# Kernel tuning notes

Hardware: AMD Instinct MI355X
Metric: run time of the kernel (lower is better)

The kernel has to match this reference:

```python
import jax, jax.numpy as jnp
import numpy as np

HID = 1024
NH = 16
HD = HID // NH  # 64
RANK = 16
B, L = 2, 2048


def setup_inputs() -> dict:
    key = jax.random.key(0)
    ks = jax.random.split(key, 9)
    s = 0.02
    return {
        "x": jax.random.normal(ks[0], (B, L, HID), dtype=jnp.float32),
        "Wq": jax.random.normal(ks[1], (HID, HID), dtype=jnp.float32) * s,
        "Wk": jax.random.normal(ks[2], (HID, HID), dtype=jnp.float32) * s,
        "Wv": jax.random.normal(ks[3], (HID, HID), dtype=jnp.float32) * s,
        "Wg": jax.random.normal(ks[4], (HID, HID), dtype=jnp.float32) * s,
        "Wgk1": jax.random.normal(ks[5], (HID, RANK), dtype=jnp.float32) * s,
        "Wgk2": jax.random.normal(ks[6], (RANK, HID), dtype=jnp.float32) * s,
        "bgk2": jnp.zeros((HID,), dtype=jnp.float32),
        "gamma": jnp.ones((HID,), dtype=jnp.float32),
        "beta": jnp.zeros((HID,), dtype=jnp.float32),
        "Wout": jax.random.normal(ks[7], (HID, HID), dtype=jnp.float32) * s,
    }


def reference(x, Wq, Wk, Wv, Wg, Wgk1, Wgk2, bgk2, gamma, beta, Wout):
    Bb, Ll, Hid = x.shape
    H, Dh = NH, HD
    # projections -> [B, L, H, Dh]
    q = (x @ Wq).reshape(Bb, Ll, H, Dh)
    k = (x @ Wk).reshape(Bb, Ll, H, Dh)
    v = (x @ Wv).reshape(Bb, Ll, H, Dh)
    gk = (jax.nn.log_sigmoid((x @ Wgk1) @ Wgk2 + bgk2) / 16.0).reshape(Bb, Ll, H, Dh)

    # time-major for scan: [L, B, H, Dh]
    qT = jnp.transpose(q, (1, 0, 2, 3))
    kT = jnp.transpose(k, (1, 0, 2, 3))
    vT = jnp.transpose(v, (1, 0, 2, 3))
    gT = jnp.transpose(gk, (1, 0, 2, 3))

    def step(state, inp):
        qt, kt, vt, gt = inp  # each [B, H, Dh]
        gate = jnp.exp(gt)
        # state[b,h,v_dim,k_dim]; gate applied along v_dim (matches torch code)
        state = state * gate[..., None] + vt[..., None] * kt[..., None, :]
        out_t = jnp.einsum('bhvk,bhk->bhv', state, qt)
        return state, out_t

    state0 = jnp.zeros((Bb, H, Dh, Dh), dtype=x.dtype)
    _, outs = jax.lax.scan(step, state0, (qT, kT, vT, gT))  # outs: [L, B, H, Dh]
    out = jnp.transpose(outs, (1, 0, 2, 3)).reshape(Bb, Ll, Hid)

    # LayerNorm over total_dim
    mu = out.mean(-1, keepdims=True)
    var = out.var(-1, keepdims=True)
    out = (out - mu) / jnp.sqrt(var + 1e-5) * gamma + beta

    # output gate + projection (dropout = identity in eval)
    out = out * jax.nn.silu(x @ Wg)
    return out @ Wout
```

## Files before the change

### kernel.cpp

```cpp
#include <hip/hip_runtime.h>
#include <cstdint>
#include <cstddef>

#define HIDS 1024
#define NHEAD 16
#define HDIM 64
#define LSEQ 2048
#define BBATCH 2
#define NROW (BBATCH * LSEQ)
#define CHUNK 64
#define NCHUNK (LSEQ / CHUNK)
#define RANK 16

typedef short short8 __attribute__((ext_vector_type(8)));
typedef float floatx4 __attribute__((ext_vector_type(4)));

__device__ __forceinline__ ushort f2bf(float f) {
  uint32_t u = __float_as_uint(f);
  uint32_t r = (u + 0x7fffu + ((u >> 16) & 1u)) >> 16;
  return (ushort)r;
}
__device__ __forceinline__ float bf2f(ushort u) {
  return __uint_as_float(((uint32_t)u) << 16);
}
__device__ __forceinline__ float logsig16(float z) {
  return (fminf(z, 0.f) - __logf(1.f + __expf(-fabsf(z)))) * (1.f / 16.f);
}

__device__ __forceinline__ void async_copy16(const void* g, void* l) {
  __builtin_amdgcn_global_load_lds(
      (const __attribute__((address_space(1))) void*)g,
      (__attribute__((address_space(3))) void*)l, 16, 0, 0);
}

__global__ __launch_bounds__(256) void prep_kernel(
    const float* __restrict__ x, ushort* __restrict__ xbf,
    const float* __restrict__ W0, const float* __restrict__ W1,
    const float* __restrict__ W2, const float* __restrict__ W3,
    const float* __restrict__ W4, ushort* __restrict__ T0,
    ushort* __restrict__ T1, ushort* __restrict__ T2, ushort* __restrict__ T3,
    ushort* __restrict__ T4) {
  __shared__ float sbuf[64 * 65];
  const int bid = blockIdx.x;
  const int tid = threadIdx.x;

  if (bid < 4096) {
    const int i = bid * 256 + tid;
    float4 f = *(const float4*)(x + (size_t)i * 4);
    ushort4 o;
    o.x = f2bf(f.x); o.y = f2bf(f.y); o.z = f2bf(f.z); o.w = f2bf(f.w);
    *(ushort4*)(xbf + (size_t)i * 4) = o;
  } else {
    const int w = bid - 4096;
    const int z = w >> 8, rem = w & 255;
    const float* W = (z == 0) ? W0 : (z == 1) ? W1 : (z == 2) ? W2
                     : (z == 3) ? W3 : W4;
    ushort* T = (z == 0) ? T0 : (z == 1) ? T1 : (z == 2) ? T2
                : (z == 3) ? T3 : T4;
    const int k0 = (rem >> 4) * 64, n0 = (rem & 15) * 64;
    const int r = tid >> 2, c4 = (tid & 3) * 16;
#pragma unroll
    for (int i = 0; i < 4; ++i) {
      float4 f = *(const float4*)(W + (size_t)(k0 + r) * HIDS + n0 + c4 + i * 4);
      sbuf[r * 65 + c4 + i * 4 + 0] = f.x;
      sbuf[r * 65 + c4 + i * 4 + 1] = f.y;
      sbuf[r * 65 + c4 + i * 4 + 2] = f.z;
      sbuf[r * 65 + c4 + i * 4 + 3] = f.w;
    }
    __syncthreads();
    const int n = tid >> 2, kc = (tid & 3) * 16;
#pragma unroll
    for (int i = 0; i < 4; ++i) {
      int kk = kc + i * 4;
      ushort4 o;
      o.x = f2bf(sbuf[(kk + 0) * 65 + n]);
      o.y = f2bf(sbuf[(kk + 1) * 65 + n]);
      o.z = f2bf(sbuf[(kk + 2) * 65 + n]);
      o.w = f2bf(sbuf[(kk + 3) * 65 + n]);
      *(ushort4*)(T + (size_t)(n0 + n) * HIDS + k0 + kk) = o;
    }
  }
}

#define XSTR 1040
__global__ __launch_bounds__(256) void xr_kernel(
    const ushort* __restrict__ xbf, const float* __restrict__ Wgk1,
    float* __restrict__ xr) {
  __shared__ float sW1[HIDS * RANK];
  __shared__ ushort sX[16 * XSTR];
  const int tid = threadIdx.x;
  const int r0 = blockIdx.x * 16;
#pragma unroll
  for (int j = 0; j < 16; ++j) {
    const int idx = j * 1024 + tid * 4;
    *(float4*)&sW1[idx] = *(const float4*)(Wgk1 + idx);
  }
#pragma unroll
  for (int j = 0; j < 8; ++j) {
    const int e = j * 2048 + tid * 8;
    const int rr = e >> 10, kk = e & 1023;
    *(short8*)&sX[rr * XSTR + kk] =
        *(const short8*)(xbf + (size_t)(r0 + rr) * HIDS + kk);
  }
  __syncthreads();
  const int r = tid >> 4, n = tid & 15;
  float acc = 0.f;
  for (int k8 = 0; k8 < HIDS; k8 += 8) {
    short8 xv = *(const short8*)&sX[r * XSTR + k8];
#pragma unroll
    for (int i = 0; i < 8; ++i)
      acc = fmaf(bf2f((ushort)xv[i]), sW1[(k8 + i) * RANK + n], acc);
  }
  xr[(size_t)(r0 + r) * RANK + n] = acc;
}

__global__ __launch_bounds__(256) void proj4_kernel(
    const ushort* __restrict__ xbf, const ushort* __restrict__ Wtq,
    const ushort* __restrict__ Wtk, const ushort* __restrict__ Wtv,
    const ushort* __restrict__ Wtg, ushort* __restrict__ qb,
    ushort* __restrict__ kb, ushort* __restrict__ vb, ushort* __restrict__ gb) {
  const int bxz = blockIdx.x;
  const int z = bxz & 3;
  const int bx = bxz >> 2;
  const ushort* Bt = (z == 0) ? Wtq : (z == 1) ? Wtk : (z == 2) ? Wtv : Wtg;
  ushort* C = (z == 0) ? qb : (z == 1) ? kb : (z == 2) ? vb : gb;
  __shared__ ushort As[2][128 * 32];
  __shared__ ushort Bs[2][128 * 32];
  const int tid = threadIdx.x;
  const int wave = tid >> 6, lane = tid & 63;
  const int wm = (wave >> 1) * 64, wn = (wave & 1) * 64;
  const int bm = blockIdx.y * 128, bn = bx * 128;
  const int lrow = tid >> 2;
  const int lk8 = ((((tid & 3) - ((tid >> 3) & 3)) & 3)) * 8;
  const ushort* Ag = xbf + (size_t)(bm + lrow) * HIDS + lk8;
  const ushort* Bg = Bt + (size_t)(bn + lrow) * HIDS + lk8;
  char* A0 = (char*)&As[0][0] + tid * 16;
  char* A1 = (char*)&As[1][0] + tid * 16;
  char* B0 = (char*)&Bs[0][0] + tid * 16;
  char* B1 = (char*)&Bs[1][0] + tid * 16;

  floatx4 acc[4][4];
#pragma unroll
  for (int i = 0; i < 4; ++i)
#pragma unroll
    for (int j = 0; j < 4; ++j) acc[i][j] = (floatx4){0.f, 0.f, 0.f, 0.f};

  const int fm = lane & 15, quad = lane >> 4;
  const int sq8 = ((quad + (fm >> 1)) & 3) * 8;

  for (int k0 = 0; k0 < HIDS; k0 += 64) {
    __syncthreads();
    async_copy16(Ag + k0, A0);
    async_copy16(Ag + (size_t)64 * HIDS + k0, A0 + 4096);
    async_copy16(Ag + k0 + 32, A1);
    async_copy16(Ag + (size_t)64 * HIDS + k0 + 32, A1 + 4096);
    async_copy16(Bg + k0, B0);
    async_copy16(Bg + (size_t)64 * HIDS + k0, B0 + 4096);
    async_copy16(Bg + k0 + 32, B1);
    async_copy16(Bg + (size_t)64 * HIDS + k0 + 32, B1 + 4096);
    __syncthreads();

#pragma unroll
    for (int ks = 0; ks < 2; ++ks) {
      short8 af[4], bfr[4];
#pragma unroll
      for (int i = 0; i < 4; ++i)
        af[i] = *(const short8*)&As[ks][(wm + i * 16 + fm) * 32 + sq8];
#pragma unroll
      for (int j = 0; j < 4; ++j)
        bfr[j] = *(const short8*)&Bs[ks][(wn + j * 16 + fm) * 32 + sq8];
#pragma unroll
      for (int i = 0; i < 4; ++i)
#pragma unroll
        for (int j = 0; j < 4; ++j)
          acc[i][j] = __builtin_amdgcn_mfma_f32_16x16x32_bf16(af[i], bfr[j],
                                                              acc[i][j], 0, 0, 0);
    }
  }

#pragma unroll
  for (int i = 0; i < 4; ++i) {
    const int row0 = bm + wm + i * 16 + quad * 4;
#pragma unroll
    for (int j = 0; j < 4; ++j) {
      const int col = bn + wn + j * 16 + fm;
#pragma unroll
      for (int r = 0; r < 4; ++r)
        C[(size_t)(row0 + r) * HIDS + col] = f2bf(acc[i][j][r]);
    }
  }
}

__global__ __launch_bounds__(256) void gemm_out_kernel(
    const ushort* __restrict__ A, const ushort* __restrict__ Bt,
    float* __restrict__ C) {
  __shared__ ushort As[2][128 * 32];
  __shared__ ushort Bs[2][128 * 32];
  const int tid = threadIdx.x;
  const int wave = tid >> 6, lane = tid & 63;
  const int wm = (wave >> 1) * 64, wn = (wave & 1) * 64;
  const int fm = lane & 15, quad = lane >> 4;
  const int sq8 = ((quad + (fm >> 1)) & 3) * 8;
  const int bm = blockIdx.y * 128, bn = blockIdx.x * 128;
  const int lrow = tid >> 2;
  const int lk8 = ((((tid & 3) - ((tid >> 3) & 3)) & 3)) * 8;
  const ushort* Ag = A + (size_t)(bm + lrow) * HIDS + lk8;
  const ushort* Bg = Bt + (size_t)(bn + lrow) * HIDS + lk8;
  char* A0 = (char*)&As[0][0] + tid * 16;
  char* A1 = (char*)&As[1][0] + tid * 16;
  char* B0 = (char*)&Bs[0][0] + tid * 16;
  char* B1 = (char*)&Bs[1][0] + tid * 16;

  floatx4 acc[4][4];
#pragma unroll
  for (int i = 0; i < 4; ++i)
#pragma unroll
    for (int j = 0; j < 4; ++j) acc[i][j] = (floatx4){0.f, 0.f, 0.f, 0.f};

  for (int k0 = 0; k0 < HIDS; k0 += 64) {
    __syncthreads();
    async_copy16(Ag + k0, A0);
    async_copy16(Ag + (size_t)64 * HIDS + k0, A0 + 4096);
    async_copy16(Ag + k0 + 32, A1);
    async_copy16(Ag + (size_t)64 * HIDS + k0 + 32, A1 + 4096);
    async_copy16(Bg + k0, B0);
    async_copy16(Bg + (size_t)64 * HIDS + k0, B0 + 4096);
    async_copy16(Bg + k0 + 32, B1);
    async_copy16(Bg + (size_t)64 * HIDS + k0 + 32, B1 + 4096);
    __syncthreads();

#pragma unroll
    for (int ks = 0; ks < 2; ++ks) {
      short8 af[4], bfr[4];
#pragma unroll
      for (int i = 0; i < 4; ++i)
        af[i] = *(const short8*)&As[ks][(wm + i * 16 + fm) * 32 + sq8];
#pragma unroll
      for (int j = 0; j < 4; ++j)
        bfr[j] = *(const short8*)&Bs[ks][(wn + j * 16 + fm) * 32 + sq8];
#pragma unroll
      for (int i = 0; i < 4; ++i)
#pragma unroll
        for (int j = 0; j < 4; ++j)
          acc[i][j] = __builtin_amdgcn_mfma_f32_16x16x32_bf16(af[i], bfr[j],
                                                              acc[i][j], 0, 0, 0);
    }
  }

#pragma unroll
  for (int i = 0; i < 4; ++i) {
    const int row0 = bm + wm + i * 16 + quad * 4;
#pragma unroll
    for (int j = 0; j < 4; ++j) {
      const int col = bn + wn + j * 16 + fm;
#pragma unroll
      for (int r = 0; r < 4; ++r)
        C[(size_t)(row0 + r) * HIDS + col] = acc[i][j][r];
    }
  }
}

#define SP 72
#define SGS 68

__global__ __launch_bounds__(256) void sdelta_kernel(
    const ushort* __restrict__ k, const ushort* __restrict__ v,
    const float* __restrict__ xr, const float* __restrict__ Wgk2,
    const float* __restrict__ bgk2, ushort* __restrict__ Sdelta,
    float* __restrict__ Lam, ushort* __restrict__ Vtg,
    ushort* __restrict__ Eb) {
  const int bid = blockIdx.x;
  const int c = bid & 31, bh = bid >> 5;
  const int b = bh >> 4, h = bh & 15;
  const int tid = threadIdx.x;
  const int lane = tid & 63, wave = tid >> 6;
  const int fm = lane & 15, quad = lane >> 4;
  const int wm2 = (wave >> 1) * 32, wn2 = (wave & 1) * 32;

  __shared__ ushort sKt[64 * SP];
  __shared__ ushort sVt[64 * SP];
  __shared__ float sG[64 * SGS];
  __shared__ float sW2[RANK * 64];

  const size_t base = ((size_t)b * LSEQ + (size_t)c * CHUNK) * HIDS + (size_t)h * HDIM;
  const int r = tid >> 2, c0 = (tid & 3) * 16;
  const size_t gb = base + (size_t)r * HIDS + c0;

  {
    const int wr = tid >> 4, wc = (tid & 15) * 4;
    *(float4*)&sW2[wr * 64 + wc] =
        *(const float4*)(Wgk2 + (size_t)wr * HIDS + h * HDIM + wc);
  }
  float xrr[16];
  {
    const size_t xrow = ((size_t)b * LSEQ + (size_t)c * CHUNK + r) * RANK;
#pragma unroll
    for (int m = 0; m < 4; ++m)
      *(float4*)&xrr[m * 4] = *(const float4*)(xr + xrow + m * 4);
  }
  float bias[16];
#pragma unroll
  for (int m = 0; m < 4; ++m)
    *(float4*)&bias[m * 4] = *(const float4*)(bgk2 + h * HDIM + c0 + m * 4);
  __syncthreads();

#pragma unroll
  for (int i = 0; i < 16; ++i) {
    float z = bias[i];
#pragma unroll
    for (int t2 = 0; t2 < 16; ++t2)
      z = fmaf(xrr[t2], sW2[t2 * 64 + c0 + i], z);
    sG[r * SGS + c0 + i] = logsig16(z);
  }
  const int pr = (tid >> 3) * 2, pc = (tid & 7) * 8;
  const size_t pb = base + (size_t)pr * HIDS + pc;
  short8 ka = *(const short8*)(k + pb);
  short8 kb2 = *(const short8*)(k + pb + HIDS);
  short8 va = *(const short8*)(v + pb);
  short8 vb2 = *(const short8*)(v + pb + HIDS);
  __syncthreads();

  const int vcol = tid & 63, qtr = tid >> 6;
  {
    float run = 0.f;
#pragma unroll
    for (int i = 0; i < 16; ++i) {
      int idx = (qtr * 16 + i) * SGS + vcol;
      run += sG[idx];
      sG[idx] = run;
    }
  }
  __syncthreads();
  float pre = 0.f;
  for (int j = 0; j < qtr; ++j) pre += sG[(j * 16 + 15) * SGS + vcol];
  __syncthreads();
#pragma unroll
  for (int i = 0; i < 16; ++i) sG[(qtr * 16 + i) * SGS + vcol] += pre;
  __syncthreads();

  {
    ushort eb[16];
#pragma unroll
    for (int i = 0; i < 16; ++i) eb[i] = f2bf(__expf(sG[r * SGS + c0 + i]));
    *(short8*)(Eb + gb) = *(short8*)&eb[0];
    *(short8*)(Eb + gb + 8) = *(short8*)&eb[8];
  }

#pragma unroll
  for (int i = 0; i < 8; ++i) {
    ushort2 kk;
    kk.x = (ushort)ka[i];
    kk.y = (ushort)kb2[i];
    *(ushort2*)&sKt[(pc + i) * SP + pr] = kk;
    float Ga = sG[pr * SGS + pc + i];
    float Gb2 = sG[(pr + 1) * SGS + pc + i];
    ushort2 vv;
    vv.x = f2bf(bf2f((ushort)va[i]) * __expf(-Ga));
    vv.y = f2bf(bf2f((ushort)vb2[i]) * __expf(-Gb2));
    *(ushort2*)&sVt[(pc + i) * SP + pr] = vv;
  }
  __syncthreads();

  {
    const size_t vb3 = (size_t)(bh * NCHUNK + c) * (HDIM * HDIM);
    *(short8*)(Vtg + vb3 + (size_t)r * HDIM + c0) = *(const short8*)&sVt[r * SP + c0];
    *(short8*)(Vtg + vb3 + (size_t)r * HDIM + c0 + 8) =
        *(const short8*)&sVt[r * SP + c0 + 8];
  }

  if (tid < 64)
    Lam[(size_t)(bh * NCHUNK + c) * HDIM + tid] = __expf(sG[63 * SGS + tid]);

  floatx4 accD[2][2];
#pragma unroll
  for (int i = 0; i < 2; ++i)
#pragma unroll
    for (int j = 0; j < 2; ++j) accD[i][j] = (floatx4){0.f, 0.f, 0.f, 0.f};
#pragma unroll
  for (int ks = 0; ks < 2; ++ks) {
    short8 av[2], bk[2];
#pragma unroll
    for (int i = 0; i < 2; ++i)
      av[i] = *(const short8*)&sVt[(wm2 + i * 16 + fm) * SP + ks * 32 + quad * 8];
#pragma unroll
    for (int j = 0; j < 2; ++j)
      bk[j] = *(const short8*)&sKt[(wn2 + j * 16 + fm) * SP + ks * 32 + quad * 8];
#pragma unroll
    for (int i = 0; i < 2; ++i)
#pragma unroll
      for (int j = 0; j < 2; ++j)
        accD[i][j] = __builtin_amdgcn_mfma_f32_16x16x32_bf16(av[i], bk[j],
                                                             accD[i][j], 0, 0, 0);
  }
  const size_t sbase = (size_t)(bh * NCHUNK + c) * (HDIM * HDIM);
#pragma unroll
  for (int i = 0; i < 2; ++i) {
    const int m0 = wm2 + i * 16 + quad * 4;
    float lam[4];
#pragma unroll
    for (int rr = 0; rr < 4; ++rr) lam[rr] = __expf(sG[63 * SGS + m0 + rr]);
#pragma unroll
    for (int j = 0; j < 2; ++j) {
      const int n = wn2 + j * 16 + fm;
#pragma unroll
      for (int rr = 0; rr < 4; ++rr)
        Sdelta[sbase + (size_t)(m0 + rr) * HDIM + n] = f2bf(accD[i][j][rr] * lam[rr]);
    }
  }
}

__global__ __launch_bounds__(256) void state_scan_kernel(
    const ushort* __restrict__ Sdelta, const float* __restrict__ Lam,
    ushort* __restrict__ Sprev) {
  const int bh = blockIdx.x >> 3;
  const int sl = blockIdx.x & 7;
  const int tid = threadIdx.x;
  const int e0 = sl * 512 + tid;
  float S0 = 0.f, S1 = 0.f;

  float pd0[2], pd1[2], pl0[2], pl1[2];
#pragma unroll
  for (int s = 0; s < 2; ++s) {
    size_t nb = (size_t)(bh * NCHUNK + s) * (HDIM * HDIM);
    size_t nl = (size_t)(bh * NCHUNK + s) * HDIM;
    pd0[s] = bf2f(Sdelta[nb + e0]);
    pd1[s] = bf2f(Sdelta[nb + e0 + 256]);
    pl0[s] = Lam[nl + (e0 >> 6)];
    pl1[s] = Lam[nl + ((e0 + 256) >> 6)];
  }

  for (int c = 0; c < NCHUNK; ++c) {
    const int s = c & 1;
    float cd0 = pd0[s], cd1 = pd1[s], cl0 = pl0[s], cl1 = pl1[s];
    if (c + 2 < NCHUNK) {
      size_t nb = (size_t)(bh * NCHUNK + c + 2) * (HDIM * HDIM);
      size_t nl = (size_t)(bh * NCHUNK + c + 2) * HDIM;
      pd0[s] = bf2f(Sdelta[nb + e0]);
      pd1[s] = bf2f(Sdelta[nb + e0 + 256]);
      pl0[s] = Lam[nl + (e0 >> 6)];
      pl1[s] = Lam[nl + ((e0 + 256) >> 6)];
    }
    size_t ob = (size_t)(bh * NCHUNK + c) * (HDIM * HDIM);
    Sprev[ob + e0] = f2bf(S0);
    Sprev[ob + e0 + 256] = f2bf(S1);
    S0 = fmaf(S0, cl0, cd0);
    S1 = fmaf(S1, cl1, cd1);
  }
}

__global__ __launch_bounds__(256) void chunk_fused_kernel(
    const ushort* __restrict__ q, const ushort* __restrict__ k,
    const ushort* __restrict__ Vtg, const ushort* __restrict__ Eb,
    const ushort* __restrict__ Sprev, ushort* __restrict__ att) {
  const int bid = blockIdx.x;
  const int c = bid & 31, bh = bid >> 5;
  const int b = bh >> 4, h = bh & 15;
  const int tid = threadIdx.x;
  const int lane = tid & 63, wave = tid >> 6;
  const int fm = lane & 15, quad = lane >> 4;
  const int wm2 = (wave >> 1) * 32, wn2 = (wave & 1) * 32;

  __shared__ ushort sQ[64 * SP];
  __shared__ ushort sK[64 * SP];
  __shared__ ushort sVt[64 * SP];
  __shared__ ushort sA[64 * SP];
  ushort* sSp = sK;

  const size_t base = ((size_t)b * LSEQ + (size_t)c * CHUNK) * HIDS + (size_t)h * HDIM;
  const size_t sbase = (size_t)(bh * NCHUNK + c) * (HDIM * HDIM);
  const int r = tid >> 2, c0 = (tid & 3) * 16;
  const size_t gb = base + (size_t)r * HIDS + c0;
  short8 sp0 = *(const short8*)(Sprev + sbase + (size_t)r * HDIM + c0);
  short8 sp1 = *(const short8*)(Sprev + sbase + (size_t)r * HDIM + c0 + 8);
  *(short8*)&sQ[r * SP + c0] = *(const short8*)(q + gb);
  *(short8*)&sQ[r * SP + c0 + 8] = *(const short8*)(q + gb + 8);
  *(short8*)&sK[r * SP + c0] = *(const short8*)(k + gb);
  *(short8*)&sK[r * SP + c0 + 8] = *(const short8*)(k + gb + 8);
  *(short8*)&sVt[r * SP + c0] = *(const short8*)(Vtg + sbase + (size_t)r * HDIM + c0);
  *(short8*)&sVt[r * SP + c0 + 8] =
      *(const short8*)(Vtg + sbase + (size_t)r * HDIM + c0 + 8);
  __syncthreads();

  floatx4 accS[2][2];
#pragma unroll
  for (int i = 0; i < 2; ++i)
#pragma unroll
    for (int j = 0; j < 2; ++j) accS[i][j] = (floatx4){0.f, 0.f, 0.f, 0.f};
#pragma unroll
  for (int ks = 0; ks < 2; ++ks) {
    short8 a[2], bb[2];
#pragma unroll
    for (int i = 0; i < 2; ++i)
      a[i] = *(const short8*)&sQ[(wm2 + i * 16 + fm) * SP + ks * 32 + quad * 8];
#pragma unroll
    for (int j = 0; j < 2; ++j)
      bb[j] = *(const short8*)&sK[(wn2 + j * 16 + fm) * SP + ks * 32 + quad * 8];
#pragma unroll
    for (int i = 0; i < 2; ++i)
#pragma unroll
      for (int j = 0; j < 2; ++j)
        accS[i][j] = __builtin_amdgcn_mfma_f32_16x16x32_bf16(a[i], bb[j],
                                                             accS[i][j], 0, 0, 0);
  }
  __syncthreads();

#pragma unroll
  for (int i = 0; i < 2; ++i)
#pragma unroll
    for (int j = 0; j < 2; ++j) {
      const int t0 = wm2 + i * 16 + quad * 4;
      const int s = wn2 + j * 16 + fm;
#pragma unroll
      for (int rr = 0; rr < 4; ++rr) {
        float val = (s <= t0 + rr) ? accS[i][j][rr] : 0.f;
        sA[(t0 + rr) * SP + s] = f2bf(val);
      }
    }
  *(short8*)&sSp[r * SP + c0] = sp0;
  *(short8*)&sSp[r * SP + c0 + 8] = sp1;
  __syncthreads();

  floatx4 acc[2][2];
#pragma unroll
  for (int i = 0; i < 2; ++i)
#pragma unroll
    for (int j = 0; j < 2; ++j) acc[i][j] = (floatx4){0.f, 0.f, 0.f, 0.f};
#pragma unroll
  for (int ks = 0; ks < 2; ++ks) {
    short8 aa[2], aq[2], bv[2], bs[2];
#pragma unroll
    for (int i = 0; i < 2; ++i) {
      aa[i] = *(const short8*)&sA[(wm2 + i * 16 + fm) * SP + ks * 32 + quad * 8];
      aq[i] = *(const short8*)&sQ[(wm2 + i * 16 + fm) * SP + ks * 32 + quad * 8];
    }
#pragma unroll
    for (int j = 0; j < 2; ++j) {
      bv[j] = *(const short8*)&sVt[(wn2 + j * 16 + fm) * SP + ks * 32 + quad * 8];
      bs[j] = *(const short8*)&sSp[(wn2 + j * 16 + fm) * SP + ks * 32 + quad * 8];
    }
#pragma unroll
    for (int i = 0; i < 2; ++i)
#pragma unroll
      for (int j = 0; j < 2; ++j) {
        acc[i][j] = __builtin_amdgcn_mfma_f32_16x16x32_bf16(aa[i], bv[j],
                                                            acc[i][j], 0, 0, 0);
        acc[i][j] = __builtin_amdgcn_mfma_f32_16x16x32_bf16(aq[i], bs[j],
                                                            acc[i][j], 0, 0, 0);
      }
  }
#pragma unroll
  for (int i = 0; i < 2; ++i)
#pragma unroll
    for (int j = 0; j < 2; ++j) {
      const int m0 = wm2 + i * 16 + quad * 4;
      const int n = wn2 + j * 16 + fm;
#pragma unroll
      for (int rr = 0; rr < 4; ++rr) {
        const size_t idx = base + (size_t)(m0 + rr) * HIDS + n;
        att[idx] = f2bf(acc[i][j][rr] * bf2f(Eb[idx]));
      }
    }
}

__global__ __launch_bounds__(256) void ln_gate_kernel(const ushort* __restrict__ att,
                                                      const ushort* __restrict__ g,
                                                      const float* __restrict__ gamma,
                                                      const float* __restrict__ beta,
                                                      ushort* __restrict__ ybf) {
  const int row = blockIdx.x;
  const int tid = threadIdx.x;
  ushort4 au = *(const ushort4*)(att + (size_t)row * HIDS + tid * 4);
  float ax = bf2f(au.x), ay = bf2f(au.y), az = bf2f(au.z), aw = bf2f(au.w);
  float s = ax + ay + az + aw;
  float ss = ax * ax + ay * ay + az * az + aw * aw;
#pragma unroll
  for (int off = 32; off; off >>= 1) {
    s += __shfl_down(s, off);
    ss += __shfl_down(ss, off);
  }
  __shared__ float rs[4], rss[4];
  const int wid = tid >> 6;
  if ((tid & 63) == 0) { rs[wid] = s; rss[wid] = ss; }
  __syncthreads();
  const float mean = (rs[0] + rs[1] + rs[2] + rs[3]) * (1.f / HIDS);
  const float ex2 = (rss[0] + rss[1] + rss[2] + rss[3]) * (1.f / HIDS);
  const float rstd = rsqrtf(ex2 - mean * mean + 1e-5f);

  float4 ga = *(const float4*)(gamma + tid * 4);
  float4 be = *(const float4*)(beta + tid * 4);
  ushort4 gu = *(const ushort4*)(g + (size_t)row * HIDS + tid * 4);
  float gx = bf2f(gu.x), gy = bf2f(gu.y), gz = bf2f(gu.z), gw = bf2f(gu.w);
  float4 o;
  o.x = ((ax - mean) * rstd * ga.x + be.x) * (gx / (1.f + __expf(-gx)));
  o.y = ((ay - mean) * rstd * ga.y + be.y) * (gy / (1.f + __expf(-gy)));
  o.z = ((az - mean) * rstd * ga.z + be.z) * (gz / (1.f + __expf(-gz)));
  o.w = ((aw - mean) * rstd * ga.w + be.w) * (gw / (1.f + __expf(-gw)));
  ushort4 ob;
  ob.x = f2bf(o.x); ob.y = f2bf(o.y); ob.z = f2bf(o.z); ob.w = f2bf(o.w);
  *(ushort4*)(ybf + (size_t)row * HIDS + tid * 4) = ob;
}

extern "C" void kernel_launch(void* const* d_in, const int* in_sizes, int n_in,
                              void* d_out, int out_size, void* d_ws, size_t ws_size,
                              hipStream_t stream) {
  const float* x     = (const float*)d_in[0];
  const float* Wq    = (const float*)d_in[1];
  const float* Wk    = (const float*)d_in[2];
  const float* Wv    = (const float*)d_in[3];
  const float* Wg    = (const float*)d_in[4];
  const float* Wgk1  = (const float*)d_in[5];
  const float* Wgk2  = (const float*)d_in[6];
  const float* bgk2  = (const float*)d_in[7];
  const float* gamma = (const float*)d_in[8];
  const float* beta  = (const float*)d_in[9];
  const float* Wout  = (const float*)d_in[10];
  float* out = (float*)d_out;

  const size_t SZ = (size_t)NROW * HIDS;
  float* ws = (float*)d_ws;
  float* Lamb = ws;
  ushort* attb   = (ushort*)(ws + 65536);
  ushort* Sdelta = attb + SZ;
  ushort* Sprevb = Sdelta + SZ;
  ushort* Vtgb   = Sprevb + SZ;
  ushort* Ebb    = Vtgb + SZ;
  ushort* qbf = Ebb + SZ;
  ushort* kbf = qbf + SZ;
  ushort* vbf = kbf + SZ;
  ushort* gbf = vbf + SZ;
  ushort* xbf = gbf + SZ;
  ushort* Wtq = xbf + SZ;
  ushort* Wtk = Wtq + HIDS * HIDS;
  ushort* Wtv = Wtk + HIDS * HIDS;
  ushort* Wtg = Wtv + HIDS * HIDS;
  ushort* Wto = Wtg + HIDS * HIDS;
  float* xrb = (float*)(Wto + HIDS * HIDS);
  ushort* ybf = vbf;

  prep_kernel<<<4096 + 1280, 256, 0, stream>>>(
      x, xbf, Wq, Wk, Wv, Wg, Wout, Wtq, Wtk, Wtv, Wtg, Wto);

  xr_kernel<<<NROW / 16, 256, 0, stream>>>(xbf, Wgk1, xrb);

  proj4_kernel<<<dim3(4 * (HIDS / 128), NROW / 128), 256, 0, stream>>>(
      xbf, Wtq, Wtk, Wtv, Wtg, qbf, kbf, vbf, gbf);

  sdelta_kernel<<<BBATCH * NHEAD * NCHUNK, 256, 0, stream>>>(
      kbf, vbf, xrb, Wgk2, bgk2, Sdelta, Lamb, Vtgb, Ebb);
  state_scan_kernel<<<256, 256, 0, stream>>>(Sdelta, Lamb, Sprevb);
  chunk_fused_kernel<<<BBATCH * NHEAD * NCHUNK, 256, 0, stream>>>(
      qbf, kbf, Vtgb, Ebb, Sprevb, attb);

  ln_gate_kernel<<<NROW, 256, 0, stream>>>(attb, gbf, gamma, beta, ybf);
  gemm_out_kernel<<<dim3(HIDS / 128, NROW / 128), 256, 0, stream>>>(ybf, Wto, out);
}
```

Before: 222.8 us.

## Rewrite QKVG projection as 256x256-tile 8-wave pipelined GEMM over concatenated weights

Replaces the four-way 128x128 projection GEMM with a single kernel that treats Wq/Wk/Wv/Wg as one contiguous 4096x1024 weight and computes 256x256 tiles with 8 waves. It double-buffers LDS tiles, issues the next k-tile's async copies in pieces interleaved with MFMA phases, uses fine-grained barriers with s_setprio around MFMA bursts, and uses explicit vmcnt waits. The larger tiles are meant to raise arithmetic intensity and the pipelining is meant to hide global loads. In exchange it uses more registers and 64KB of LDS per block, and it relies on the weight and output buffers being contiguous in memory.

```diff
diff --git a/kernel.cpp b/kernel.cpp
--- a/kernel.cpp
+++ b/kernel.cpp
@@ -114,81 +114,176 @@
   xr[(size_t)(r0 + r) * RANK + n] = acc;
 }
 
-__global__ __launch_bounds__(256) void proj4_kernel(
-    const ushort* __restrict__ xbf, const ushort* __restrict__ Wtq,
-    const ushort* __restrict__ Wtk, const ushort* __restrict__ Wtv,
-    const ushort* __restrict__ Wtg, ushort* __restrict__ qb,
-    ushort* __restrict__ kb, ushort* __restrict__ vb, ushort* __restrict__ gb) {
-  const int bxz = blockIdx.x;
-  const int z = bxz & 3;
-  const int bx = bxz >> 2;
-  const ushort* Bt = (z == 0) ? Wtq : (z == 1) ? Wtk : (z == 2) ? Wtv : Wtg;
-  ushort* C = (z == 0) ? qb : (z == 1) ? kb : (z == 2) ? vb : gb;
-  __shared__ ushort As[2][128 * 32];
-  __shared__ ushort Bs[2][128 * 32];
+#define POFF(buf, mat, half) ((((buf)*2 + (mat)) * 2 + (half)) * 8192)
+
+__global__ __launch_bounds__(512, 2) void proj8_kernel(
+    const ushort* __restrict__ xbf, const ushort* __restrict__ Wcat,
+    ushort* __restrict__ Cq) {
+  __shared__ ushort sT[2 * 2 * 2 * 8192];
   const int tid = threadIdx.x;
-  const int wave = tid >> 6, lane = tid & 63;
-  const int wm = (wave >> 1) * 64, wn = (wave & 1) * 64;
-  const int bm = blockIdx.y * 128, bn = bx * 128;
-  const int lrow = tid >> 2;
-  const int lk8 = ((((tid & 3) - ((tid >> 3) & 3)) & 3)) * 8;
-  const ushort* Ag = xbf + (size_t)(bm + lrow) * HIDS + lk8;
-  const ushort* Bg = Bt + (size_t)(bn + lrow) * HIDS + lk8;
-  char* A0 = (char*)&As[0][0] + tid * 16;
-  char* A1 = (char*)&As[1][0] + tid * 16;
-  char* B0 = (char*)&Bs[0][0] + tid * 16;
-  char* B1 = (char*)&Bs[1][0] + tid * 16;
-
-  floatx4 acc[4][4];
-#pragma unroll
-  for (int i = 0; i < 4; ++i)
-#pragma unroll
-    for (int j = 0; j < 4; ++j) acc[i][j] = (floatx4){0.f, 0.f, 0.f, 0.f};
-
+  const int lane = tid & 63, wid = tid >> 6;
   const int fm = lane & 15, quad = lane >> 4;
   const int sq8 = ((quad + (fm >> 1)) & 3) * 8;
-
-  for (int k0 = 0; k0 < HIDS; k0 += 64) {
-    __syncthreads();
-    async_copy16(Ag + k0, A0);
-    async_copy16(Ag + (size_t)64 * HIDS + k0, A0 + 4096);
-    async_copy16(Ag + k0 + 32, A1);
-    async_copy16(Ag + (size_t)64 * HIDS + k0 + 32, A1 + 4096);
-    async_copy16(Bg + k0, B0);
-    async_copy16(Bg + (size_t)64 * HIDS + k0, B0 + 4096);
-    async_copy16(Bg + k0 + 32, B1);
-    async_copy16(Bg + (size_t)64 * HIDS + k0 + 32, B1 + 4096);
-    __syncthreads();
-
-#pragma unroll
-    for (int ks = 0; ks < 2; ++ks) {
-      short8 af[4], bfr[4];
-#pragma unroll
-      for (int i = 0; i < 4; ++i)
-        af[i] = *(const short8*)&As[ks][(wm + i * 16 + fm) * 32 + sq8];
-#pragma unroll
-      for (int j = 0; j < 4; ++j)
-        bfr[j] = *(const short8*)&Bs[ks][(wn + j * 16 + fm) * 32 + sq8];
-#pragma unroll
-      for (int i = 0; i < 4; ++i)
-#pragma unroll
-        for (int j = 0; j < 4; ++j)
-          acc[i][j] = __builtin_amdgcn_mfma_f32_16x16x32_bf16(af[i], bfr[j],
-                                                              acc[i][j], 0, 0, 0);
-    }
-  }
-
-#pragma unroll
-  for (int i = 0; i < 4; ++i) {
-    const int row0 = bm + wm + i * 16 + quad * 4;
-#pragma unroll
-    for (int j = 0; j < 4; ++j) {
-      const int col = bn + wn + j * 16 + fm;
-#pragma unroll
-      for (int r = 0; r < 4; ++r)
-        C[(size_t)(row0 + r) * HIDS + col] = f2bf(acc[i][j][r]);
-    }
-  }
+  const int wr = wid >> 2, wc = wid & 3;
+  const int bm = blockIdx.y * 256, bn = blockIdx.x * 256;
+
+  const int srow = tid >> 2;
+  const int qch = ((((tid & 3) - ((tid >> 3) & 3)) & 3)) * 8;
+  const ushort* Ab = xbf + (size_t)(bm + srow) * HIDS + qch;
+  const ushort* Bb = Wcat + (size_t)(bn + srow) * HIDS + qch;
+
+#define STAGE_A(ktn, nb)                                                      \
+  do {                                                                        \
+    const int kc_ = (ktn) * 64;                                               \
+    async_copy16(Ab + kc_, (char*)&sT[POFF(nb, 0, 0)] + tid * 16);            \
+    async_copy16(Ab + (size_t)128 * HIDS + kc_,                               \
+                 (char*)&sT[POFF(nb, 0, 0)] + tid * 16 + 8192);               \
+    async_copy16(Ab + kc_ + 32, (char*)&sT[POFF(nb, 0, 1)] + tid * 16);       \
+    async_copy16(Ab + (size_t)128 * HIDS + kc_ + 32,                          \
+                 (char*)&sT[POFF(nb, 0, 1)] + tid * 16 + 8192);               \
+  } while (0)
+#define STAGE_B0(ktn, nb)                                                     \
+  do {                                                                        \
+    const int kc_ = (ktn) * 64;                                               \
+    async_copy16(Bb + kc_, (char*)&sT[POFF(nb, 1, 0)] + tid * 16);            \
+    async_copy16(Bb + (size_t)128 * HIDS + kc_,                               \
+                 (char*)&sT[POFF(nb, 1, 0)] + tid * 16 + 8192);               \
+  } while (0)
+#define STAGE_B1(ktn, nb)                                                     \
+  do {                                                                        \
+    const int kc_ = (ktn) * 64;                                               \
+    async_copy16(Bb + kc_ + 32, (char*)&sT[POFF(nb, 1, 1)] + tid * 16);       \
+    async_copy16(Bb + (size_t)128 * HIDS + kc_ + 32,                          \
+                 (char*)&sT[POFF(nb, 1, 1)] + tid * 16 + 8192);               \
+  } while (0)
+#define BARRIER()                        \
+  do {                                   \
+    asm volatile("" ::: "memory");       \
+    __builtin_amdgcn_s_barrier();        \
+    asm volatile("" ::: "memory");       \
+  } while (0)
+
+  const int aoff = (wr * 128 + fm) * 32 + sq8;
+  const int boff = (wc * 64 + fm) * 32 + sq8;
+
+  floatx4 acc[8][4];
+#pragma unroll
+  for (int i = 0; i < 8; ++i)
+#pragma unroll
+    for (int j = 0; j < 4; ++j) acc[i][j] = (floatx4){0.f, 0.f, 0.f, 0.f};
+
+  STAGE_A(0, 0);
+  STAGE_B0(0, 0);
+  STAGE_B1(0, 0);
+
+  for (int kt = 0; kt < 16; ++kt) {
+    const int cur = kt & 1, nxt = cur ^ 1;
+    if (kt < 15) {
+      STAGE_A(kt + 1, nxt);
+      asm volatile("s_waitcnt vmcnt(4)" ::: "memory");
+    } else {
+      asm volatile("s_waitcnt vmcnt(0)" ::: "memory");
+    }
+    BARRIER();
+
+    short8 af[4][2], bfr[4][2];
+#pragma unroll
+    for (int m = 0; m < 4; ++m) {
+      af[m][0] = *(const short8*)&sT[POFF(cur, 0, 0) + aoff + m * 512];
+      af[m][1] = *(const short8*)&sT[POFF(cur, 0, 1) + aoff + m * 512];
+    }
+#pragma unroll
+    for (int n = 0; n < 2; ++n) {
+      bfr[n][0] = *(const short8*)&sT[POFF(cur, 1, 0) + boff + n * 512];
+      bfr[n][1] = *(const short8*)&sT[POFF(cur, 1, 1) + boff + n * 512];
+    }
+    if (kt < 15) STAGE_B0(kt + 1, nxt);
+    BARRIER();
+    __builtin_amdgcn_s_setprio(1);
+#pragma unroll
+    for (int m = 0; m < 4; ++m)
+#pragma unroll
+      for (int n = 0; n < 2; ++n) {
+        acc[m][n] = __builtin_amdgcn_mfma_f32_16x16x32_bf16(af[m][0], bfr[n][0],
+                                                            acc[m][n], 0, 0, 0);
+        acc[m][n] = __builtin_amdgcn_mfma_f32_16x16x32_bf16(af[m][1], bfr[n][1],
+                                                            acc[m][n], 0, 0, 0);
+      }
+    __builtin_amdgcn_s_setprio(0);
+    BARRIER();
+
+#pragma unroll
+    for (int n = 2; n < 4; ++n) {
+      bfr[n][0] = *(const short8*)&sT[POFF(cur, 1, 0) + boff + n * 512];
+      bfr[n][1] = *(const short8*)&sT[POFF(cur, 1, 1) + boff + n * 512];
+    }
+    if (kt < 15) STAGE_B1(kt + 1, nxt);
+    BARRIER();
+    __builtin_amdgcn_s_setprio(1);
+#pragma unroll
+    for (int m = 0; m < 4; ++m)
+#pragma unroll
+      for (int n = 2; n < 4; ++n) {
+        acc[m][n] = __builtin_amdgcn_mfma_f32_16x16x32_bf16(af[m][0], bfr[n][0],
+                                                            acc[m][n], 0, 0, 0);
+        acc[m][n] = __builtin_amdgcn_mfma_f32_16x16x32_bf16(af[m][1], bfr[n][1],
+                                                            acc[m][n], 0, 0, 0);
+      }
+    __builtin_amdgcn_s_setprio(0);
+    BARRIER();
+
+#pragma unroll
+    for (int m = 0; m < 4; ++m) {
+      af[m][0] = *(const short8*)&sT[POFF(cur, 0, 0) + aoff + (m + 4) * 512];
+      af[m][1] = *(const short8*)&sT[POFF(cur, 0, 1) + aoff + (m + 4) * 512];
+    }
+    BARRIER();
+    __builtin_amdgcn_s_setprio(1);
+#pragma unroll
+    for (int m = 0; m < 4; ++m)
+#pragma unroll
+      for (int n = 0; n < 2; ++n) {
+        acc[m + 4][n] = __builtin_amdgcn_mfma_f32_16x16x32_bf16(
+            af[m][0], bfr[n][0], acc[m + 4][n], 0, 0, 0);
+        acc[m + 4][n] = __builtin_amdgcn_mfma_f32_16x16x32_bf16(
+            af[m][1], bfr[n][1], acc[m + 4][n], 0, 0, 0);
+      }
+    __builtin_amdgcn_s_setprio(0);
+    BARRIER();
+
+    __builtin_amdgcn_s_setprio(1);
+#pragma unroll
+    for (int m = 0; m < 4; ++m)
+#pragma unroll
+      for (int n = 2; n < 4; ++n) {
+        acc[m + 4][n] = __builtin_amdgcn_mfma_f32_16x16x32_bf16(
+            af[m][0], bfr[n][0], acc[m + 4][n], 0, 0, 0);
+        acc[m + 4][n] = __builtin_amdgcn_mfma_f32_16x16x32_bf16(
+            af[m][1], bfr[n][1], acc[m + 4][n], 0, 0, 0);
+      }
+    __builtin_amdgcn_s_setprio(0);
+    BARRIER();
+  }
+
+  const int cb = bn + wc * 64;
+  const int z = cb >> 10;
+  const int ccol = cb & 1023;
+  ushort* C = Cq + (size_t)z * ((size_t)NROW * HIDS);
+#pragma unroll
+  for (int m = 0; m < 8; ++m) {
+    const int row0 = bm + wr * 128 + m * 16 + quad * 4;
+#pragma unroll
+    for (int n = 0; n < 4; ++n) {
+      const int col = ccol + n * 16 + fm;
+#pragma unroll
+      for (int rr = 0; rr < 4; ++rr)
+        C[(size_t)(row0 + rr) * HIDS + col] = f2bf(acc[m][n][rr]);
+    }
+  }
+#undef STAGE_A
+#undef STAGE_B0
+#undef STAGE_B1
+#undef BARRIER
 }
 
 __global__ __launch_bounds__(256) void gemm_out_kernel(
@@ -642,8 +737,7 @@
 
   xr_kernel<<<NROW / 16, 256, 0, stream>>>(xbf, Wgk1, xrb);
 
-  proj4_kernel<<<dim3(4 * (HIDS / 128), NROW / 128), 256, 0, stream>>>(
-      xbf, Wtq, Wtk, Wtv, Wtg, qbf, kbf, vbf, gbf);
+  proj8_kernel<<<dim3(NROW / 256, NROW / 256), 512, 0, stream>>>(xbf, Wtq, qbf);
 
   sdelta_kernel<<<BBATCH * NHEAD * NCHUNK, 256, 0, stream>>>(
       kbf, vbf, xrb, Wgk2, bgk2, Sdelta, Lamb, Vtgb, Ebb);
```

Result: no change. 219.2 us (-1.6%).
